# Kernel optimization log

Measured on AMD Instinct MI355X. Metric: run time of the kernel, lower is better.

The kernel has to match this reference:

```python
import jax, jax.numpy as jnp
import numpy as np

EXTENT = 3.0            # 'radius' arg of the model is passed as extents to ContinuousConv
SEARCH_R = EXTENT / 2.0 # Open3D fixed_radius_search uses extents/2
KS = 6                  # kernel_size [6,6,6]
N, K = 10000, 32
EPS = 1e-12
FOUR_OVER_PI = float(4.0 / np.pi)


def ball_to_cube_volume_preserving(u):
    # u: [...,3] in the unit ball -> cube [-1,1]^3 (Open3D mapping:
    # MapSphereToCylinder followed by MapCylinderToCube).
    x, y, z = u[..., 0], u[..., 1], u[..., 2]
    sq = x * x + y * y + z * z
    norm = jnp.sqrt(jnp.maximum(sq, EPS))
    rho2 = x * x + y * y
    # sphere -> cylinder (volume preserving, two regions)
    in_cone = 1.25 * z * z > rho2
    s1 = jnp.sqrt(3.0 * norm / (norm + jnp.abs(z)))
    s2 = norm / jnp.sqrt(jnp.maximum(rho2, EPS))
    s = jnp.where(in_cone, s1, s2)
    xc = x * s
    yc = y * s
    zc = jnp.where(in_cone, jnp.sign(z) * norm, 1.5 * z)
    tiny = sq < EPS
    xc = jnp.where(tiny, 0.0, xc)
    yc = jnp.where(tiny, 0.0, yc)
    zc = jnp.where(tiny, 0.0, zc)
    # cylinder -> cube (inverse concentric / Shirley-Chiu map on xy disc)
    sq_xy = xc * xc + yc * yc
    norm_xy = jnp.sqrt(jnp.maximum(sq_xy, EPS))
    x_major = jnp.abs(yc) <= jnp.abs(xc)
    xd = jnp.where(jnp.abs(xc) < EPS, 1.0, xc)
    yd = jnp.where(jnp.abs(yc) < EPS, 1.0, yc)
    tx = jnp.sign(xc) * norm_xy
    ty = jnp.sign(yc) * norm_xy
    xq = jnp.where(x_major, tx, ty * FOUR_OVER_PI * jnp.arctan(xc / yd))
    yq = jnp.where(x_major, tx * FOUR_OVER_PI * jnp.arctan(yc / xd), ty)
    tiny_xy = sq_xy < EPS
    xq = jnp.where(tiny_xy, 0.0, xq)
    yq = jnp.where(tiny_xy, 0.0, yq)
    return jnp.stack([xq, yq, zc], axis=-1)


def continuous_conv(feats, pos, nidx, nmask, W, b):
    # feats [N,Cin], pos [N,3], nidx [N,K] int32 (padded), nmask [N,K] bool
    # W [KS,KS,KS,Cin,Cout], b [Cout]
    n, k = nidx.shape
    Cin, Cout = W.shape[3], W.shape[4]
    M = KS * KS * KS
    maskf = nmask.astype(feats.dtype)
    u = (pos[nidx] - pos[:, None, :]) * (2.0 / EXTENT)          # [N,K,3], unit ball
    coords = (ball_to_cube_volume_preserving(u) + 1.0) * (0.5 * (KS - 1))  # align_corners
    i0f = jnp.floor(coords)
    frac = coords - i0f
    i0 = jnp.clip(i0f.astype(jnp.int32), 0, KS - 1)
    i1 = jnp.minimum(i0 + 1, KS - 1)
    fN = feats[nidx]                                            # [N,K,Cin]
    base = jnp.arange(n, dtype=jnp.int32)[:, None] * M          # [N,1]
    # Scatter trilinear-weighted neighbor features into per-point kernel cells:
    # A[j, cell, :] = sum_{neighbors k, corners c} w_{j,k,c} * feats[nidx[j,k]]
    A = jnp.zeros((n * M, Cin), feats.dtype)
    for cx in (0, 1):
        ix = i1[..., 0] if cx else i0[..., 0]
        wx = frac[..., 0] if cx else 1.0 - frac[..., 0]
        for cy in (0, 1):
            iy = i1[..., 1] if cy else i0[..., 1]
            wy = frac[..., 1] if cy else 1.0 - frac[..., 1]
            for cz in (0, 1):
                iz = i1[..., 2] if cz else i0[..., 2]
                wz = frac[..., 2] if cz else 1.0 - frac[..., 2]
                w = wx * wy * wz * maskf                        # [N,K]
                flat = (base + (ix * KS + iy) * KS + iz).reshape(-1)
                A = A.at[flat].add((w[..., None] * fN).reshape(n * k, Cin))
    out = jnp.einsum('nmc,mco->no', A.reshape(n, M, Cin), W.reshape(M, Cin, Cout))
    # normalize=True (Open3D default): divide by neighbor count, guarded for empty
    cnt = maskf.sum(axis=1, keepdims=True)
    out = jnp.where(cnt > 0, out / jnp.maximum(cnt, 1.0), out)
    return jax.nn.relu(out + b)                                 # use_bias + activation


def setup_inputs() -> dict:
    rng = np.random.default_rng(0)
    L = 16.0  # box side -> ~32 neighbors on average within SEARCH_R
    pos = (rng.random((N, 3)) * L).astype(np.float32)
    nidx = np.zeros((N, K), np.int32)
    nmask = np.zeros((N, K), bool)
    chunk = 512
    for s in range(0, N, chunk):
        d2 = ((pos[s:s + chunk, None, :] - pos[None, :, :]) ** 2).sum(-1)
        part = np.argpartition(d2, K, axis=1)[:, :K].astype(np.int32)
        m = np.take_along_axis(d2, part, axis=1) <= SEARCH_R * SEARCH_R
        nidx[s:s + chunk] = np.where(m, part, 0)
        nmask[s:s + chunk] = m

    def p(*shape):
        return jnp.asarray((rng.standard_normal(shape) * 0.1).astype(np.float32))

    return {
        'feats': jnp.asarray(rng.standard_normal((N, 4)).astype(np.float32)),
        'pos': jnp.asarray(pos),
        'neighbor_idx': jnp.asarray(nidx),
        'neighbor_mask': jnp.asarray(nmask),
        'W1': p(KS, KS, KS, 4, 64), 'b1': jnp.zeros((64,), jnp.float32),
        'W2': p(KS, KS, KS, 64, 64), 'b2': jnp.zeros((64,), jnp.float32),
        'W3': p(KS, KS, KS, 64, 32), 'b3': jnp.zeros((32,), jnp.float32),
        'Wfc1': p(32, 64), 'bfc1': jnp.zeros((64,), jnp.float32),
        'Wfc2': p(64, 64), 'bfc2': jnp.zeros((64,), jnp.float32),
        'Wfc3': p(64, 32), 'bfc3': jnp.zeros((32,), jnp.float32),
        'Wout': p(32, 3), 'bout': jnp.zeros((3,), jnp.float32),
    }


def reference(feats, pos, neighbor_idx, neighbor_mask, W1, b1, W2, b2, W3, b3,
              Wfc1, bfc1, Wfc2, bfc2, Wfc3, bfc3, Wout, bout):
    x = continuous_conv(feats, pos, neighbor_idx, neighbor_mask, W1, b1)
    x = continuous_conv(x, pos, neighbor_idx, neighbor_mask, W2, b2)
    x = continuous_conv(x, pos, neighbor_idx, neighbor_mask, W3, b3)
    x = jax.nn.relu(x @ Wfc1 + bfc1)
    x = jax.nn.relu(x @ Wfc2 + bfc2)
    x = jax.nn.relu(x @ Wfc3 + bfc3)
    return x @ Wout + bout
```

## Files before the change

kernel.cpp:

```cpp
#include <hip/hip_runtime.h>
#include <math.h>

#define NPTS  10000
#define KNB   32
#define NCELL 216
#define NSGT  157

__device__ __forceinline__ float sgnf(float v) {
    return (v > 0.0f) ? 1.0f : ((v < 0.0f) ? -1.0f : 0.0f);
}

__device__ __forceinline__ void ball_to_cube(float x, float y, float z,
                                             float& X, float& Y, float& Z) {
    const float EPSF = 1e-12f;
    const float FOPI = (float)(4.0 / 3.14159265358979323846);
    float sq   = x * x + y * y + z * z;
    float norm = sqrtf(fmaxf(sq, EPSF));
    float rho2 = x * x + y * y;
    bool in_cone = (1.25f * z * z > rho2);
    float s1 = sqrtf(3.0f * norm / (norm + fabsf(z)));
    float s2 = norm / sqrtf(fmaxf(rho2, EPSF));
    float s  = in_cone ? s1 : s2;
    float xc = x * s;
    float yc = y * s;
    float zc = in_cone ? sgnf(z) * norm : 1.5f * z;
    if (sq < EPSF) { xc = 0.0f; yc = 0.0f; zc = 0.0f; }
    float sq_xy   = xc * xc + yc * yc;
    float norm_xy = sqrtf(fmaxf(sq_xy, EPSF));
    bool x_major = (fabsf(yc) <= fabsf(xc));
    float xd = (fabsf(xc) < EPSF) ? 1.0f : xc;
    float yd = (fabsf(yc) < EPSF) ? 1.0f : yc;
    float tx = sgnf(xc) * norm_xy;
    float ty = sgnf(yc) * norm_xy;
    float xq = x_major ? tx : ty * FOPI * atanf(xc / yd);
    float yq = x_major ? tx * FOPI * atanf(yc / xd) : ty;
    if (sq_xy < EPSF) { xq = 0.0f; yq = 0.0f; }
    X = xq; Y = yq; Z = zc;
}

__global__ __launch_bounds__(256) void geom_kernel(
    const float* __restrict__ pos, const int* __restrict__ nidx,
    uint4* __restrict__ geo, float* __restrict__ cnt) {
    int t = blockIdx.x * 256 + threadIdx.x;
    if (t >= NPTS * KNB) return;
    int j = t >> 5;
    int k = t & 31;
    int nid = nidx[t];
    float px = pos[j * 3], py = pos[j * 3 + 1], pz = pos[j * 3 + 2];
    float qx = pos[nid * 3], qy = pos[nid * 3 + 1], qz = pos[nid * 3 + 2];
    float dx = __fsub_rn(px, qx), dy = __fsub_rn(py, qy), dz = __fsub_rn(pz, qz);
    float d2 = __fadd_rn(__fadd_rn(__fmul_rn(dx, dx), __fmul_rn(dy, dy)),
                         __fmul_rn(dz, dz));
    bool valid = (d2 <= 2.25f);
    if (valid && nid == 0) {
        for (int kk = 0; kk < k; ++kk) {
            if (nidx[j * KNB + kk] == 0) { valid = false; break; }
        }
    }
    uint4 g = make_uint4(0u, 0u, 0u, 0u);
    if (valid) {
        const float C = (float)(2.0 / 3.0);
        float ux = (qx - px) * C, uy = (qy - py) * C, uz = (qz - pz) * C;
        float X, Y, Z;
        ball_to_cube(ux, uy, uz, X, Y, Z);
        float cs[3] = { (X + 1.0f) * 2.5f, (Y + 1.0f) * 2.5f, (Z + 1.0f) * 2.5f };
        int i0[3], i1[3];
        float fr[3];
        #pragma unroll
        for (int d = 0; d < 3; ++d) {
            float f0 = floorf(cs[d]);
            fr[d] = cs[d] - f0;
            int a = (int)f0;
            a = min(max(a, 0), 5);
            i0[d] = a;
            i1[d] = min(a + 1, 5);
        }
        int c000 = (i0[0] * 6 + i0[1]) * 6 + i0[2];
        unsigned bits = (unsigned)c000
                      | ((unsigned)(i1[0] - i0[0]) << 8)
                      | ((unsigned)(i1[1] - i0[1]) << 9)
                      | ((unsigned)(i1[2] - i0[2]) << 10)
                      | (1u << 11)
                      | ((unsigned)nid << 12);
        g.x = __float_as_uint(fr[0]);
        g.y = __float_as_uint(fr[1]);
        g.z = __float_as_uint(fr[2]);
        g.w = bits;
        atomicAdd(&cnt[j], 1.0f);
    }
    geo[t] = g;
}

__global__ __launch_bounds__(256) void sort_kernel(
    const uint4* __restrict__ geo, uint2* __restrict__ contribs,
    int* __restrict__ starts) {
    __shared__ int hist[13824];
    __shared__ int part[257];
    const int sg = blockIdx.x, tid = threadIdx.x;
    for (int i = tid; i < 13824; i += 256) hist[i] = 0;
    __syncthreads();
    const int npts = min(64, NPTS - sg * 64);
    const int nrec = npts * KNB;
    const uint4* gb = geo + (size_t)sg * 64 * KNB;
    for (int r = tid; r < nrec; r += 256) {
        uint4 g = gb[r];
        if (g.w & 2048u) {
            int ptl = r >> 5;
            int c000 = g.w & 255u;
            int dxo = (g.w & 256u)  ? 36 : 0;
            int dyo = (g.w & 512u)  ? 6  : 0;
            int dzo = (g.w & 1024u) ? 1  : 0;
            #pragma unroll
            for (int c = 0; c < 8; ++c) {
                int cell = c000 + ((c & 4) ? dxo : 0) + ((c & 2) ? dyo : 0)
                                + ((c & 1) ? dzo : 0);
                atomicAdd(&hist[cell * 64 + ptl], 1);
            }
        }
    }
    __syncthreads();
    int sum = 0;
    for (int j = 0; j < 54; ++j) sum += hist[tid * 54 + j];
    part[tid] = sum;
    __syncthreads();
    if (tid == 0) {
        int run = 0;
        for (int i = 0; i < 256; ++i) { int v = part[i]; part[i] = run; run += v; }
        part[256] = run;
    }
    __syncthreads();
    {
        int run = part[tid];
        for (int j = 0; j < 54; ++j) {
            int i = tid * 54 + j;
            int v = hist[i]; hist[i] = run; run += v;
        }
    }
    __syncthreads();
    for (int i = tid; i < 864; i += 256)
        starts[sg * 865 + i] = hist[(i >> 2) * 64 + (i & 3) * 16];
    if (tid == 0) starts[sg * 865 + 864] = part[256];
    __syncthreads();
    uint2* cb = contribs + (size_t)sg * 16384;
    for (int r = tid; r < nrec; r += 256) {
        uint4 g = gb[r];
        if (g.w & 2048u) {
            int ptl = r >> 5;
            float fx = __uint_as_float(g.x);
            float fy = __uint_as_float(g.y);
            float fz = __uint_as_float(g.z);
            int c000 = g.w & 255u;
            int dxo = (g.w & 256u)  ? 36 : 0;
            int dyo = (g.w & 512u)  ? 6  : 0;
            int dzo = (g.w & 1024u) ? 1  : 0;
            int nid = (g.w >> 12) & 16383u;
            unsigned pay = (unsigned)nid | ((unsigned)ptl << 14);
            #pragma unroll
            for (int c = 0; c < 8; ++c) {
                float wgt = ((c & 4) ? fx : 1.f - fx)
                          * ((c & 2) ? fy : 1.f - fy)
                          * ((c & 1) ? fz : 1.f - fz);
                int cell = c000 + ((c & 4) ? dxo : 0) + ((c & 2) ? dyo : 0)
                                + ((c & 1) ? dzo : 0);
                int p = atomicAdd(&hist[cell * 64 + ptl], 1);
                cb[p] = make_uint2(__float_as_uint(wgt), pay);
            }
        }
    }
}

template<int CIN, int COUT, int CPC, int MT, int KSPLIT>
__global__ __launch_bounds__(256, 2) void conv_kernel(
    const float* __restrict__ feats, const float* __restrict__ W,
    const uint2* __restrict__ contribs, const int* __restrict__ starts,
    float* __restrict__ partial) {
    constexpr int KC   = CPC * CIN;
    constexpr int ASTR = KC + 4;
    constexpr int CG   = COUT / 4;
    constexpr int NSG  = MT / 64;
    constexpr int NCHUNK = NCELL / CPC;
    constexpr int NWG  = (NSG == 2) ? 2 : 1;
    constexpr int WPT  = (KC * COUT) / 1024;
    constexpr int RPW  = MT / 4;

    __shared__ alignas(16) float Al[MT * ASTR];
    __shared__ alignas(16) float Wl[2][KC * COUT];
    __shared__ int Sl[NSG][868];

    const int tid  = threadIdx.x;
    const int lane = tid & 63;
    const int wv   = tid >> 6;
    const int cg   = tid % CG;
    const int pg   = tid / CG;
    const int bx   = blockIdx.x;
    const int ks   = blockIdx.y;

    for (int s = 0; s < NSG; ++s) {
        int sg = bx * NSG + s;
        for (int i = tid; i < 865; i += 256)
            Sl[s][i] = (sg < NSGT) ? starts[sg * 865 + i] : 0;
    }
    __syncthreads();

    const int c0 = NCHUNK * ks / KSPLIT;
    const int c1 = NCHUNK * (ks + 1) / KSPLIT;

    const int sgl = (NSG == 2) ? (wv >> 1) : 0;
    const int wg0 = (NSG == 2) ? ((wv & 1) * 2) : wv;
    const uint2* cb = contribs + (size_t)(bx * NSG + sgl) * 16384;

    auto stage = [&](int c) {
        float4 z4; z4.x = z4.y = z4.z = z4.w = 0.f;
        float4* Az = reinterpret_cast<float4*>(Al + wv * RPW * ASTR);
        for (int i = lane; i < RPW * (ASTR / 4); i += 64) Az[i] = z4;
        const int cellbase = c * CPC;
        for (int cl = 0; cl < CPC; ++cl) {
            const int m = cellbase + cl;
            const int key = m * 4 + wg0;
            int s = Sl[sgl][key];
            int e = Sl[sgl][key + NWG];
            if (s >= e) continue;
            const int kb = cl * CIN;
            float vacc = 0.f;
            int prevpt = -1;
            int i = s;
            while (i < e) {
                int n2 = min(64, e - i);
                uint2 rec = make_uint2(0u, 0u);
                if (lane < n2) rec = cb[i + lane];
                for (int t = 0; t < n2; ++t) {
                    float wgt = __shfl(__uint_as_float(rec.x), t);
                    int pay   = __shfl((int)rec.y, t);
                    int ptl = (pay >> 14) & 63;
                    if (ptl != prevpt) {
                        if (prevpt >= 0 && lane < CIN)
                            Al[(sgl * 64 + prevpt) * ASTR + kb + lane] = vacc;
                        vacc = 0.f;
                        prevpt = ptl;
                    }
                    int nid = pay & 16383;
                    float f = (lane < CIN) ? feats[(size_t)nid * CIN + lane] : 0.f;
                    vacc = fmaf(wgt, f, vacc);
                }
                i += n2;
            }
            if (prevpt >= 0 && lane < CIN)
                Al[(sgl * 64 + prevpt) * ASTR + kb + lane] = vacc;
        }
    };

    {
        const float4* Wg = reinterpret_cast<const float4*>(W + (size_t)c0 * KC * COUT);
        float4* Wd = reinterpret_cast<float4*>(Wl[0]);
        for (int i = tid; i < KC * COUT / 4; i += 256) Wd[i] = Wg[i];
    }
    stage(c0);
    __syncthreads();

    float4 acc[4];
    #pragma unroll
    for (int p = 0; p < 4; ++p) { acc[p].x = acc[p].y = acc[p].z = acc[p].w = 0.f; }

    for (int c = c0; c < c1; ++c) {
        const int b = (c - c0) & 1;
        float4 wpre[WPT];
        if (c + 1 < c1) {
            const float4* Wg = reinterpret_cast<const float4*>(W + (size_t)(c + 1) * KC * COUT);
            #pragma unroll
            for (int j = 0; j < WPT; ++j) wpre[j] = Wg[tid + j * 256];
        }
        const float* Wb = Wl[b];
        #pragma unroll 2
        for (int g = 0; g < KC / 4; ++g) {
            float4 wf[4];
            #pragma unroll
            for (int j = 0; j < 4; ++j)
                wf[j] = *reinterpret_cast<const float4*>(Wb + (g * 4 + j) * COUT + cg * 4);
            float4 af[4];
            #pragma unroll
            for (int p = 0; p < 4; ++p)
                af[p] = *reinterpret_cast<const float4*>(Al + (pg * 4 + p) * ASTR + g * 4);
            #pragma unroll
            for (int p = 0; p < 4; ++p) {
                const float* afp = reinterpret_cast<const float*>(&af[p]);
                #pragma unroll
                for (int j = 0; j < 4; ++j) {
                    float a = afp[j];
                    acc[p].x = fmaf(a, wf[j].x, acc[p].x);
                    acc[p].y = fmaf(a, wf[j].y, acc[p].y);
                    acc[p].z = fmaf(a, wf[j].z, acc[p].z);
                    acc[p].w = fmaf(a, wf[j].w, acc[p].w);
                }
            }
        }
        __syncthreads();
        if (c + 1 < c1) {
            float4* Wd = reinterpret_cast<float4*>(Wl[b ^ 1]);
            #pragma unroll
            for (int j = 0; j < WPT; ++j) Wd[tid + j * 256] = wpre[j];
            stage(c + 1);
        }
        __syncthreads();
    }

    #pragma unroll
    for (int p = 0; p < 4; ++p) {
        int n = bx * MT + pg * 4 + p;
        if (n < NPTS)
            *reinterpret_cast<float4*>(partial + ((size_t)ks * NPTS + n) * COUT + cg * 4) = acc[p];
    }
}

template<int COUT, int KSPLIT>
__global__ __launch_bounds__(256) void combine_kernel(
    const float* __restrict__ partial, const float* __restrict__ cnt,
    const float* __restrict__ bias, float* __restrict__ out) {
    int idx = blockIdx.x * 256 + threadIdx.x;
    if (idx >= NPTS * COUT) return;
    int n = idx / COUT, co = idx % COUT;
    float s = 0.f;
    #pragma unroll
    for (int k2 = 0; k2 < KSPLIT; ++k2)
        s += partial[((size_t)k2 * NPTS + n) * COUT + co];
    float c = cnt[n];
    if (c > 0.f) s /= fmaxf(c, 1.f);
    out[idx] = fmaxf(s + bias[co], 0.f);
}

__global__ __launch_bounds__(64) void fc_kernel(
    const float* __restrict__ x,
    const float* __restrict__ W1, const float* __restrict__ b1,
    const float* __restrict__ W2, const float* __restrict__ b2,
    const float* __restrict__ W3, const float* __restrict__ b3,
    const float* __restrict__ W4, const float* __restrict__ b4,
    float* __restrict__ out) {
    int n = blockIdx.x;
    int lane = threadIdx.x;
    float xv = (lane < 32) ? x[(size_t)n * 32 + lane] : 0.0f;

    float t = b1[lane];
    for (int ci = 0; ci < 32; ++ci)
        t = fmaf(__shfl(xv, ci), W1[ci * 64 + lane], t);
    float h1 = fmaxf(t, 0.0f);

    t = b2[lane];
    for (int ci = 0; ci < 64; ++ci)
        t = fmaf(__shfl(h1, ci), W2[ci * 64 + lane], t);
    float h2 = fmaxf(t, 0.0f);

    int l32 = lane & 31;
    t = b3[l32];
    for (int ci = 0; ci < 64; ++ci)
        t = fmaf(__shfl(h2, ci), W3[ci * 32 + l32], t);
    float h3 = fmaxf(t, 0.0f);

    int ch = (lane < 3) ? lane : 0;
    float o = b4[ch];
    for (int ci = 0; ci < 32; ++ci)
        o = fmaf(__shfl(h3, ci), W4[ci * 3 + ch], o);
    if (lane < 3) out[(size_t)n * 3 + lane] = o;
}

extern "C" void kernel_launch(void* const* d_in, const int* in_sizes, int n_in,
                              void* d_out, int out_size, void* d_ws, size_t ws_size,
                              hipStream_t stream) {
    const float* feats = (const float*)d_in[0];
    const float* pos   = (const float*)d_in[1];
    const int*   nidx  = (const int*)d_in[2];
    const float* W1 = (const float*)d_in[4];
    const float* b1 = (const float*)d_in[5];
    const float* W2 = (const float*)d_in[6];
    const float* b2 = (const float*)d_in[7];
    const float* W3 = (const float*)d_in[8];
    const float* b3 = (const float*)d_in[9];
    const float* Wfc1 = (const float*)d_in[10];
    const float* bfc1 = (const float*)d_in[11];
    const float* Wfc2 = (const float*)d_in[12];
    const float* bfc2 = (const float*)d_in[13];
    const float* Wfc3 = (const float*)d_in[14];
    const float* bfc3 = (const float*)d_in[15];
    const float* Wout = (const float*)d_in[16];
    const float* bout = (const float*)d_in[17];

    char* ws = (char*)d_ws;
    uint4* geo     = (uint4*)(ws);
    uint2* contrib = (uint2*)(ws + 5120000);
    float* partial = (float*)(ws + 25698304);
    float* x1      = (float*)(ws + 30818304);
    float* x2      = (float*)(ws + 33378304);
    float* x3      = (float*)(ws + 35938304);
    float* cnt     = (float*)(ws + 37218304);
    int*   starts  = (int*)  (ws + 37258304);

    hipMemsetAsync(cnt, 0, NPTS * sizeof(float), stream);
    geom_kernel<<<(NPTS * KNB) / 256, 256, 0, stream>>>(pos, nidx, geo, cnt);
    sort_kernel<<<NSGT, 256, 0, stream>>>(geo, contrib, starts);

    conv_kernel<4, 64, 8, 64, 2><<<dim3(157, 2), 256, 0, stream>>>(
        feats, W1, contrib, starts, partial);
    combine_kernel<64, 2><<<(NPTS * 64 + 255) / 256, 256, 0, stream>>>(
        partial, cnt, b1, x1);

    conv_kernel<64, 64, 1, 64, 2><<<dim3(157, 2), 256, 0, stream>>>(
        x1, W2, contrib, starts, partial);
    combine_kernel<64, 2><<<(NPTS * 64 + 255) / 256, 256, 0, stream>>>(
        partial, cnt, b2, x2);

    conv_kernel<64, 32, 1, 128, 4><<<dim3(79, 4), 256, 0, stream>>>(
        x2, W3, contrib, starts, partial);
    combine_kernel<32, 4><<<(NPTS * 32 + 255) / 256, 256, 0, stream>>>(
        partial, cnt, b3, x3);

    fc_kernel<<<NPTS, 64, 0, stream>>>(x3, Wfc1, bfc1, Wfc2, bfc2,
                                       Wfc3, bfc3, Wout, bout, (float*)d_out);
}
```

Before: 2.288 ms.

## Sort contributions per cell only and gather with LDS atomics in conv staging

The sort kernel now builds a 216-bin histogram per cell instead of a per-cell-per-point histogram, and it packs the cell index into each contribution record. The conv staging step drops the serial per-wave shuffle loop and lets every thread process records independently, accumulating float4 feature slices into the LDS A-tile with shared-memory atomics. Launch bounds are raised to three blocks per CU, the second conv is split four ways, and the workspace is laid out so partial buffers alias the geometry buffer. This trades sequential gather latency for LDS atomic contention and a larger partial-sum combine.

```diff
diff --git a/kernel.cpp b/kernel.cpp
--- a/kernel.cpp
+++ b/kernel.cpp
@@ -94,10 +94,10 @@
 __global__ __launch_bounds__(256) void sort_kernel(
     const uint4* __restrict__ geo, uint2* __restrict__ contribs,
     int* __restrict__ starts) {
-    __shared__ int hist[13824];
-    __shared__ int part[257];
+    __shared__ int hist[NCELL];
+    __shared__ int pref[NCELL + 1];
     const int sg = blockIdx.x, tid = threadIdx.x;
-    for (int i = tid; i < 13824; i += 256) hist[i] = 0;
+    if (tid < NCELL) hist[tid] = 0;
     __syncthreads();
     const int npts = min(64, NPTS - sg * 64);
     const int nrec = npts * KNB;
@@ -105,7 +105,6 @@
     for (int r = tid; r < nrec; r += 256) {
         uint4 g = gb[r];
         if (g.w & 2048u) {
-            int ptl = r >> 5;
             int c000 = g.w & 255u;
             int dxo = (g.w & 256u)  ? 36 : 0;
             int dyo = (g.w & 512u)  ? 6  : 0;
@@ -114,32 +113,20 @@
             for (int c = 0; c < 8; ++c) {
                 int cell = c000 + ((c & 4) ? dxo : 0) + ((c & 2) ? dyo : 0)
                                 + ((c & 1) ? dzo : 0);
-                atomicAdd(&hist[cell * 64 + ptl], 1);
+                atomicAdd(&hist[cell], 1);
             }
         }
     }
-    __syncthreads();
-    int sum = 0;
-    for (int j = 0; j < 54; ++j) sum += hist[tid * 54 + j];
-    part[tid] = sum;
     __syncthreads();
     if (tid == 0) {
         int run = 0;
-        for (int i = 0; i < 256; ++i) { int v = part[i]; part[i] = run; run += v; }
-        part[256] = run;
-    }
-    __syncthreads();
-    {
-        int run = part[tid];
-        for (int j = 0; j < 54; ++j) {
-            int i = tid * 54 + j;
-            int v = hist[i]; hist[i] = run; run += v;
-        }
-    }
-    __syncthreads();
-    for (int i = tid; i < 864; i += 256)
-        starts[sg * 865 + i] = hist[(i >> 2) * 64 + (i & 3) * 16];
-    if (tid == 0) starts[sg * 865 + 864] = part[256];
+        for (int m = 0; m < NCELL; ++m) { pref[m] = run; run += hist[m]; }
+        pref[NCELL] = run;
+    }
+    __syncthreads();
+    for (int i = tid; i < NCELL + 1; i += 256)
+        starts[sg * (NCELL + 1) + i] = pref[i];
+    if (tid < NCELL) hist[tid] = pref[tid];
     __syncthreads();
     uint2* cb = contribs + (size_t)sg * 16384;
     for (int r = tid; r < nrec; r += 256) {
@@ -154,7 +141,6 @@
             int dyo = (g.w & 512u)  ? 6  : 0;
             int dzo = (g.w & 1024u) ? 1  : 0;
             int nid = (g.w >> 12) & 16383u;
-            unsigned pay = (unsigned)nid | ((unsigned)ptl << 14);
             #pragma unroll
             for (int c = 0; c < 8; ++c) {
                 float wgt = ((c & 4) ? fx : 1.f - fx)
@@ -162,15 +148,17 @@
                           * ((c & 1) ? fz : 1.f - fz);
                 int cell = c000 + ((c & 4) ? dxo : 0) + ((c & 2) ? dyo : 0)
                                 + ((c & 1) ? dzo : 0);
-                int p = atomicAdd(&hist[cell * 64 + ptl], 1);
-                cb[p] = make_uint2(__float_as_uint(wgt), pay);
+                int p = atomicAdd(&hist[cell], 1);
+                cb[p] = make_uint2(__float_as_uint(wgt),
+                                   (unsigned)nid | ((unsigned)ptl << 14)
+                                                 | ((unsigned)cell << 20));
             }
         }
     }
 }
 
 template<int CIN, int COUT, int CPC, int MT, int KSPLIT>
-__global__ __launch_bounds__(256, 2) void conv_kernel(
+__global__ __launch_bounds__(256, 3) void conv_kernel(
     const float* __restrict__ feats, const float* __restrict__ W,
     const uint2* __restrict__ contribs, const int* __restrict__ starts,
     float* __restrict__ partial) {
@@ -179,80 +167,66 @@
     constexpr int CG   = COUT / 4;
     constexpr int NSG  = MT / 64;
     constexpr int NCHUNK = NCELL / CPC;
-    constexpr int NWG  = (NSG == 2) ? 2 : 1;
     constexpr int WPT  = (KC * COUT) / 1024;
-    constexpr int RPW  = MT / 4;
+    constexpr int TPC  = CIN / 4;
+    constexpr int GPB  = 256 / TPC;
 
     __shared__ alignas(16) float Al[MT * ASTR];
     __shared__ alignas(16) float Wl[2][KC * COUT];
-    __shared__ int Sl[NSG][868];
-
-    const int tid  = threadIdx.x;
-    const int lane = tid & 63;
-    const int wv   = tid >> 6;
-    const int cg   = tid % CG;
-    const int pg   = tid / CG;
-    const int bx   = blockIdx.x;
-    const int ks   = blockIdx.y;
-
-    for (int s = 0; s < NSG; ++s) {
-        int sg = bx * NSG + s;
-        for (int i = tid; i < 865; i += 256)
-            Sl[s][i] = (sg < NSGT) ? starts[sg * 865 + i] : 0;
-    }
-    __syncthreads();
+    __shared__ int Sl[NSG][NCELL + 1];
+
+    const int tid   = threadIdx.x;
+    const int cg    = tid % CG;
+    const int pg    = tid / CG;
+    const int bx    = blockIdx.x;
+    const int ks    = blockIdx.y;
+    const int gslot = tid / TPC;
+    const int ch    = tid % TPC;
+
+    for (int s2 = 0; s2 < NSG; ++s2) {
+        int sg = bx * NSG + s2;
+        for (int i = tid; i < NCELL + 1; i += 256)
+            Sl[s2][i] = (sg < NSGT) ? starts[sg * (NCELL + 1) + i] : 0;
+    }
 
     const int c0 = NCHUNK * ks / KSPLIT;
     const int c1 = NCHUNK * (ks + 1) / KSPLIT;
 
-    const int sgl = (NSG == 2) ? (wv >> 1) : 0;
-    const int wg0 = (NSG == 2) ? ((wv & 1) * 2) : wv;
-    const uint2* cb = contribs + (size_t)(bx * NSG + sgl) * 16384;
-
     auto stage = [&](int c) {
         float4 z4; z4.x = z4.y = z4.z = z4.w = 0.f;
-        float4* Az = reinterpret_cast<float4*>(Al + wv * RPW * ASTR);
-        for (int i = lane; i < RPW * (ASTR / 4); i += 64) Az[i] = z4;
+        float4* Az = reinterpret_cast<float4*>(Al);
+        #pragma unroll 4
+        for (int i = tid; i < MT * (ASTR / 4); i += 256) Az[i] = z4;
+        __syncthreads();
         const int cellbase = c * CPC;
-        for (int cl = 0; cl < CPC; ++cl) {
-            const int m = cellbase + cl;
-            const int key = m * 4 + wg0;
-            int s = Sl[sgl][key];
-            int e = Sl[sgl][key + NWG];
-            if (s >= e) continue;
-            const int kb = cl * CIN;
-            float vacc = 0.f;
-            int prevpt = -1;
-            int i = s;
-            while (i < e) {
-                int n2 = min(64, e - i);
-                uint2 rec = make_uint2(0u, 0u);
-                if (lane < n2) rec = cb[i + lane];
-                for (int t = 0; t < n2; ++t) {
-                    float wgt = __shfl(__uint_as_float(rec.x), t);
-                    int pay   = __shfl((int)rec.y, t);
-                    int ptl = (pay >> 14) & 63;
-                    if (ptl != prevpt) {
-                        if (prevpt >= 0 && lane < CIN)
-                            Al[(sgl * 64 + prevpt) * ASTR + kb + lane] = vacc;
-                        vacc = 0.f;
-                        prevpt = ptl;
-                    }
-                    int nid = pay & 16383;
-                    float f = (lane < CIN) ? feats[(size_t)nid * CIN + lane] : 0.f;
-                    vacc = fmaf(wgt, f, vacc);
-                }
-                i += n2;
+        #pragma unroll
+        for (int s2 = 0; s2 < NSG; ++s2) {
+            const uint2* cbs = contribs + (size_t)(bx * NSG + s2) * 16384;
+            const int s = Sl[s2][cellbase];
+            const int e = Sl[s2][cellbase + CPC];
+            for (int i = s + gslot; i < e; i += GPB) {
+                uint2 rec = cbs[i];
+                float wgt = __uint_as_float(rec.x);
+                int nid = rec.y & 16383;
+                int ptl = (rec.y >> 14) & 63;
+                int cel = (rec.y >> 20);
+                float4 f4 = *reinterpret_cast<const float4*>(
+                    feats + (size_t)nid * CIN + ch * 4);
+                float* dst = Al + (s2 * 64 + ptl) * ASTR
+                           + (cel - cellbase) * CIN + ch * 4;
+                atomicAdd(dst + 0, wgt * f4.x);
+                atomicAdd(dst + 1, wgt * f4.y);
+                atomicAdd(dst + 2, wgt * f4.z);
+                atomicAdd(dst + 3, wgt * f4.w);
             }
-            if (prevpt >= 0 && lane < CIN)
-                Al[(sgl * 64 + prevpt) * ASTR + kb + lane] = vacc;
         }
     };
 
     {
         const float4* Wg = reinterpret_cast<const float4*>(W + (size_t)c0 * KC * COUT);
         float4* Wd = reinterpret_cast<float4*>(Wl[0]);
-        for (int i = tid; i < KC * COUT / 4; i += 256) Wd[i] = Wg[i];
+        #pragma unroll
+        for (int j = 0; j < WPT; ++j) Wd[tid + j * 256] = Wg[tid + j * 256];
     }
     stage(c0);
     __syncthreads();
@@ -383,14 +357,14 @@
     const float* bout = (const float*)d_in[17];
 
     char* ws = (char*)d_ws;
-    uint4* geo     = (uint4*)(ws);
-    uint2* contrib = (uint2*)(ws + 5120000);
-    float* partial = (float*)(ws + 25698304);
-    float* x1      = (float*)(ws + 30818304);
-    float* x2      = (float*)(ws + 33378304);
-    float* x3      = (float*)(ws + 35938304);
-    float* cnt     = (float*)(ws + 37218304);
-    int*   starts  = (int*)  (ws + 37258304);
+    uint2* contrib = (uint2*)(ws);
+    int*   starts  = (int*)  (ws + 20578304);
+    float* cnt     = (float*)(ws + 20714624);
+    float* x1      = (float*)(ws + 20754624);
+    float* x2      = (float*)(ws + 23314624);
+    float* x3      = (float*)(ws + 25874624);
+    uint4* geo     = (uint4*)(ws + 27154624);
+    float* partial = (float*)(ws + 27154624);
 
     hipMemsetAsync(cnt, 0, NPTS * sizeof(float), stream);
     geom_kernel<<<(NPTS * KNB) / 256, 256, 0, stream>>>(pos, nidx, geo, cnt);
@@ -401,9 +375,9 @@
     combine_kernel<64, 2><<<(NPTS * 64 + 255) / 256, 256, 0, stream>>>(
         partial, cnt, b1, x1);
 
-    conv_kernel<64, 64, 1, 64, 2><<<dim3(157, 2), 256, 0, stream>>>(
+    conv_kernel<64, 64, 1, 64, 4><<<dim3(157, 4), 256, 0, stream>>>(
         x1, W2, contrib, starts, partial);
-    combine_kernel<64, 2><<<(NPTS * 64 + 255) / 256, 256, 0, stream>>>(
+    combine_kernel<64, 4><<<(NPTS * 64 + 255) / 256, 256, 0, stream>>>(
         partial, cnt, b2, x2);
 
     conv_kernel<64, 32, 1, 128, 4><<<dim3(79, 4), 256, 0, stream>>>(
```

Result: slower. 2.580 ms (+12.8%).
